# Kernel optimization log

Measured on AMD Instinct MI355X. Metric: run time of the kernel, lower is better.

## Reference

```python
import jax, jax.numpy as jnp
import numpy as np

N = 8192
IN_F = 256
OUT_F = 256


def setup_inputs() -> dict:
    key = jax.random.key(0)
    k_v, k_adj, k1, k2, k3, kb = jax.random.split(key, 6)
    stdv = 1.0 / np.sqrt(OUT_F)
    V = jax.random.normal(k_v, (N, IN_F), dtype=jnp.float32)
    adj = jax.random.randint(k_adj, (N, N), 0, 4, dtype=jnp.int32)
    w1 = jax.random.uniform(k1, (IN_F, OUT_F), jnp.float32, -stdv, stdv)
    w2 = jax.random.uniform(k2, (IN_F, OUT_F), jnp.float32, -stdv, stdv)
    w3 = jax.random.uniform(k3, (IN_F, OUT_F), jnp.float32, -stdv, stdv)
    bias = jax.random.uniform(kb, (OUT_F,), jnp.float32, -stdv, stdv)
    return {"V": V, "adj": adj, "w1": w1, "w2": w2, "w3": w3, "bias": bias}


def reference(V, adj, w1, w2, w3, bias):
    # typed relational GCN: for each edge type k in {1,2,3},
    # aggregate (adj==k) @ (V @ wk), then sum and add bias
    o1 = jnp.matmul((adj == 1).astype(jnp.float32), jnp.matmul(V, w1))
    o2 = jnp.matmul((adj == 2).astype(jnp.float32), jnp.matmul(V, w2))
    o3 = jnp.matmul((adj == 3).astype(jnp.float32), jnp.matmul(V, w3))
    return o1 + o2 + o3 + bias
```

## Files before the change

kernel.cpp:

```cpp
#include <hip/hip_runtime.h>

typedef __attribute__((ext_vector_type(4))) float f32x4;
typedef __attribute__((ext_vector_type(16))) float f32x16;
typedef __attribute__((ext_vector_type(4))) unsigned short u16x4;
typedef __attribute__((ext_vector_type(4))) int i32x4;
typedef __attribute__((ext_vector_type(8))) __bf16 bf16x8;

union FragAB {
  u16x4 u[2];
  i32x4 v;
  bf16x8 f;
};

static __device__ __forceinline__ unsigned short f2bf(float x) {
  union { float f; unsigned u; } v;
  v.f = x;
  unsigned r = v.u + 0x7FFFu + ((v.u >> 16) & 1u);
  return (unsigned short)(r >> 16);
}

#define NN 8192

__global__ __launch_bounds__(256) void k_prep(
    const int* __restrict__ adj, const float* __restrict__ V,
    const float* __restrict__ w1, const float* __restrict__ w2,
    const float* __restrict__ w3, const float* __restrict__ bias,
    unsigned char* __restrict__ adj2b, unsigned short* __restrict__ Vbp,
    unsigned short* __restrict__ Wbp, float* __restrict__ out) {
  int t = blockIdx.x * 256 + threadIdx.x;
  int nT = gridDim.x * 256;
  for (int g = t; g < 16777216; g += nT) {
    i32x4 a = *(const i32x4*)(adj + (size_t)g * 4);
    adj2b[g] = (unsigned char)((a.x & 3) | ((a.y & 3) << 2) |
                               ((a.z & 3) << 4) | ((a.w & 3) << 6));
  }
  for (int g = t; g < 524288; g += nT) {
    int f = g * 4;
    int row = f >> 8, kcol = f & 255;
    f32x4 x = *(const f32x4*)(V + (size_t)f);
    u16x4 h;
    h.x = f2bf(x.x); h.y = f2bf(x.y); h.z = f2bf(x.z); h.w = f2bf(x.w);
    *(u16x4*)(Vbp + (size_t)(kcol >> 3) * 65536 + (size_t)row * 8 + (kcol & 7)) = h;
  }
  for (int e = t; e < 65536; e += nT) {
    int k = e >> 8, n = e & 255;
    Wbp[(size_t)(k >> 3) * 6144 + (size_t)(0 * 256 + n) * 8 + (k & 7)] = f2bf(w1[e]);
  }
  for (int e = t; e < 65536; e += nT) {
    int k = e >> 8, n = e & 255;
    Wbp[(size_t)(k >> 3) * 6144 + (size_t)(1 * 256 + n) * 8 + (k & 7)] = f2bf(w2[e]);
  }
  for (int e = t; e < 65536; e += nT) {
    int k = e >> 8, n = e & 255;
    Wbp[(size_t)(k >> 3) * 6144 + (size_t)(2 * 256 + n) * 8 + (k & 7)] = f2bf(w3[e]);
  }
  for (int g = t; g < 524288; g += nT) {
    *(f32x4*)(out + (size_t)g * 4) = *(const f32x4*)(bias + ((g * 4) & 255));
  }
}

__global__ __launch_bounds__(256) void k_transform(
    const unsigned short* __restrict__ Vbp, const unsigned short* __restrict__ Wbp,
    unsigned short* __restrict__ Bp) {
  int bx = blockIdx.x;
  int rb = bx & 127, nb = bx >> 7;
  int tid = threadIdx.x, lane = tid & 63;
  int wv = tid >> 6;
  int wr = wv >> 1, wc = wv & 1;
  int q = lane >> 4, l16 = lane & 15;

  f32x4 acc[2][4];
#pragma unroll
  for (int i = 0; i < 2; i++)
#pragma unroll
    for (int j = 0; j < 4; j++) acc[i][j] = (f32x4)0.0f;

  int r0 = rb * 64 + wr * 32 + l16;
  int n0 = nb * 128 + wc * 64 + l16;
  const unsigned short* av = Vbp + (size_t)q * 65536 + (size_t)r0 * 8;
  const unsigned short* bv = Wbp + (size_t)q * 6144 + (size_t)n0 * 8;

#pragma unroll 2
  for (int kk = 0; kk < 256; kk += 32) {
    FragAB af[2], bf[4];
#pragma unroll
    for (int mt = 0; mt < 2; mt++)
      af[mt].v = *(const i32x4*)(av + (size_t)(kk >> 3) * 65536 + mt * 128);
#pragma unroll
    for (int nt = 0; nt < 4; nt++)
      bf[nt].v = *(const i32x4*)(bv + (size_t)(kk >> 3) * 6144 + nt * 128);
#pragma unroll
    for (int mt = 0; mt < 2; mt++)
#pragma unroll
      for (int nt = 0; nt < 4; nt++)
        acc[mt][nt] = __builtin_amdgcn_mfma_f32_16x16x32_bf16(
            af[mt].f, bf[nt].f, acc[mt][nt], 0, 0, 0);
  }
#pragma unroll
  for (int mt = 0; mt < 2; mt++)
#pragma unroll
    for (int nt = 0; nt < 4; nt++) {
      int n = n0 + nt * 16;
      int ty = n >> 8, nn = n & 255;
      int j0 = rb * 64 + wr * 32 + mt * 16 + q * 4;
      u16x4 hv;
      hv.x = f2bf(acc[mt][nt].x);
      hv.y = f2bf(acc[mt][nt].y);
      hv.z = f2bf(acc[mt][nt].z);
      hv.w = f2bf(acc[mt][nt].w);
      size_t idx = (size_t)ty * 2097152 + (size_t)(j0 >> 4) * 4096 + nn * 16 + (j0 & 15);
      *(u16x4*)(Bp + idx) = hv;
    }
}

__global__ __launch_bounds__(256, 2) void k_agg(const unsigned* __restrict__ adj2,
                                                const unsigned short* __restrict__ Bp,
                                                float* __restrict__ out) {
  int bx = blockIdx.x;
  int ks = bx & 7, rb = bx >> 3;
  int tid = threadIdx.x, lane = tid & 63;
  int wv = tid >> 6;
  int q = lane >> 5, l32 = lane & 31;
  int qsh = q << 4;

  __shared__ unsigned short ldsB[2][12288];

  f32x16 acc[8];
#pragma unroll
  for (int nt = 0; nt < 8; nt++) acc[nt] = (f32x16)0.0f;

  int row = rb * 128 + wv * 32 + l32;
  const unsigned* ap = adj2 + (size_t)row * 512 + ks * 64;

  const char* Bpb = (const char*)Bp;
  const char* sp[6];
#pragma unroll
  for (int c = 0; c < 6; c++) {
    int ty = c >> 1;
    sp[c] = Bpb + (size_t)ty * 4194304 + (size_t)ks * 524288 + (c & 1) * 4096 +
            tid * 16;
  }

  i32x4 rg[6];
#pragma unroll
  for (int c = 0; c < 6; c++) rg[c] = *(const i32x4*)sp[c];
#pragma unroll
  for (int c = 0; c < 6; c++)
    *(i32x4*)&ldsB[0][c * 2048 + tid * 8] = rg[c];
  unsigned cw = ap[0];
  __syncthreads();

  for (int s = 0; s < 64; ++s) {
    int cur = s & 1;
    if (s < 63) {
#pragma unroll
      for (int c = 0; c < 6; c++)
        rg[c] = *(const i32x4*)(sp[c] + (size_t)(s + 1) * 8192);
    }
    unsigned nxc = (s < 63) ? ap[s + 1] : 0u;
    unsigned w = cw >> qsh;
#pragma unroll
    for (int ty = 0; ty < 3; ty++) {
      FragAB bv[8];
#pragma unroll
      for (int nt = 0; nt < 8; nt++)
        bv[nt].v = *(const i32x4*)&ldsB[cur][ty * 4096 + (nt * 32 + l32) * 16 + q * 8];
      FragAB A;
#pragma unroll
      for (int d = 0; d < 4; d++) {
        unsigned p0 = (w >> (4 * d)) & 3u, p1 = (w >> (4 * d + 2)) & 3u;
        A.v[d] = (int)((p0 == (unsigned)(ty + 1) ? 0x3F80u : 0u) |
                       (p1 == (unsigned)(ty + 1) ? 0x3F800000u : 0u));
      }
#pragma unroll
      for (int nt = 0; nt < 8; nt++)
        acc[nt] = __builtin_amdgcn_mfma_f32_32x32x16_bf16(A.f, bv[nt].f,
                                                          acc[nt], 0, 0, 0);
    }
    if (s < 63) {
#pragma unroll
      for (int c = 0; c < 6; c++)
        *(i32x4*)&ldsB[cur ^ 1][c * 2048 + tid * 8] = rg[c];
    }
    cw = nxc;
    __syncthreads();
  }
#pragma unroll
  for (int nt = 0; nt < 8; nt++) {
    int col = nt * 32 + l32;
    int rowb = rb * 128 + wv * 32 + 4 * q;
#pragma unroll
    for (int r = 0; r < 16; r++) {
      int orow = rowb + (r & 3) + 8 * (r >> 2);
      atomicAdd(out + (size_t)orow * 256 + col, acc[nt][r]);
    }
  }
}

extern "C" void kernel_launch(void* const* d_in, const int* in_sizes, int n_in,
                              void* d_out, int out_size, void* d_ws,
                              size_t ws_size, hipStream_t stream) {
  const float* V = (const float*)d_in[0];
  const int* adj = (const int*)d_in[1];
  const float* w1 = (const float*)d_in[2];
  const float* w2 = (const float*)d_in[3];
  const float* w3 = (const float*)d_in[4];
  const float* bias = (const float*)d_in[5];
  float* out = (float*)d_out;
  unsigned short* Bp = (unsigned short*)d_ws;
  unsigned char* adj2b = (unsigned char*)d_ws + 0xC00000;
  unsigned short* Vbp = (unsigned short*)((char*)d_ws + 0x1C00000);
  unsigned short* Wbp = (unsigned short*)((char*)d_ws + 0x2000000);

  k_prep<<<dim3(2048), dim3(256), 0, stream>>>(adj, V, w1, w2, w3, bias, adj2b,
                                               Vbp, Wbp, out);
  k_transform<<<dim3(768), dim3(256), 0, stream>>>(Vbp, Wbp, Bp);
  k_agg<<<dim3(512), dim3(256), 0, stream>>>((const unsigned*)adj2b, Bp, out);
}
```

Before: 510.2 us.

## Repartition aggregation warps by output columns and pad LDS layout

```diff
diff --git a/kernel.cpp b/kernel.cpp
--- a/kernel.cpp
+++ b/kernel.cpp
@@ -119,82 +119,115 @@
   int bx = blockIdx.x;
   int ks = bx & 7, rb = bx >> 3;
   int tid = threadIdx.x, lane = tid & 63;
-  int wv = tid >> 6;
+  int wn = tid >> 6;
   int q = lane >> 5, l32 = lane & 31;
   int qsh = q << 4;
 
-  __shared__ unsigned short ldsB[2][12288];
-
-  f32x16 acc[8];
-#pragma unroll
-  for (int nt = 0; nt < 8; nt++) acc[nt] = (f32x16)0.0f;
-
-  int row = rb * 128 + wv * 32 + l32;
-  const unsigned* ap = adj2 + (size_t)row * 512 + ks * 64;
+  __shared__ unsigned short ldsB[2][3][256][24];
+
+  f32x16 acc[4][2];
+#pragma unroll
+  for (int mt = 0; mt < 4; mt++)
+#pragma unroll
+    for (int nt = 0; nt < 2; nt++) acc[mt][nt] = (f32x16)0.0f;
+
+  const unsigned* ap = adj2 + (size_t)(rb * 128 + l32) * 512 + ks * 64;
 
   const char* Bpb = (const char*)Bp;
   const char* sp[6];
 #pragma unroll
-  for (int c = 0; c < 6; c++) {
-    int ty = c >> 1;
-    sp[c] = Bpb + (size_t)ty * 4194304 + (size_t)ks * 524288 + (c & 1) * 4096 +
-            tid * 16;
-  }
+  for (int c = 0; c < 6; c++)
+    sp[c] = Bpb + (size_t)(c >> 1) * 4194304 + (size_t)ks * 524288 +
+            (size_t)(c & 1) * 4096 + (size_t)tid * 16;
+
+#define AGG_MT(CC, MT, BV0, BV1, HI)                                           \
+  {                                                                            \
+    unsigned w = (unsigned)(HI ? (CC >> 32) : CC) >> qsh;                      \
+    FragAB A;                                                                  \
+    _Pragma("unroll") for (int d = 0; d < 4; d++) {                            \
+      unsigned p0 = (w >> (4 * d)) & 3u, p1 = (w >> (4 * d + 2)) & 3u;         \
+      A.v[d] = (int)((p0 == ty1 ? 0x3F80u : 0u) |                              \
+                     (p1 == ty1 ? 0x3F800000u : 0u));                          \
+    }                                                                          \
+    acc[MT][0] = __builtin_amdgcn_mfma_f32_32x32x16_bf16(A.f, BV0.f,           \
+                                                         acc[MT][0], 0, 0, 0); \
+    acc[MT][1] = __builtin_amdgcn_mfma_f32_32x32x16_bf16(A.f, BV1.f,           \
+                                                         acc[MT][1], 0, 0, 0); \
+  }
+
+#define AGG_TY(BUF, TY, HI)                                                    \
+  {                                                                            \
+    const unsigned ty1 = TY + 1;                                               \
+    FragAB bv0, bv1;                                                           \
+    bv0.v = *(const i32x4*)&ldsB[BUF][TY][wn * 64 + l32][q * 8];               \
+    bv1.v = *(const i32x4*)&ldsB[BUF][TY][wn * 64 + 32 + l32][q * 8];          \
+    AGG_MT(cc0, 0, bv0, bv1, HI)                                               \
+    AGG_MT(cc1, 1, bv0, bv1, HI)                                               \
+    AGG_MT(cc2, 2, bv0, bv1, HI)                                               \
+    AGG_MT(cc3, 3, bv0, bv1, HI)                                               \
+  }
+
+#define AGG_STEP(BUF, HI)                                                      \
+  AGG_TY(BUF, 0, HI) AGG_TY(BUF, 1, HI) AGG_TY(BUF, 2, HI)
+
+#define AGG_STAGE_WRITE(BUF)                                                   \
+  _Pragma("unroll") for (int c = 0; c < 6; c++)                                \
+      *(i32x4*)&ldsB[BUF][c >> 1][(c & 1) * 128 + (tid >> 1)][(tid & 1) * 8] = \
+          rg[c];
 
   i32x4 rg[6];
 #pragma unroll
   for (int c = 0; c < 6; c++) rg[c] = *(const i32x4*)sp[c];
-#pragma unroll
-  for (int c = 0; c < 6; c++)
-    *(i32x4*)&ldsB[0][c * 2048 + tid * 8] = rg[c];
-  unsigned cw = ap[0];
+  AGG_STAGE_WRITE(0)
+  unsigned long long cc0 = *(const unsigned long long*)(ap);
+  unsigned long long cc1 = *(const unsigned long long*)(ap + 16384);
+  unsigned long long cc2 = *(const unsigned long long*)(ap + 32768);
+  unsigned long long cc3 = *(const unsigned long long*)(ap + 49152);
   __syncthreads();
 
-  for (int s = 0; s < 64; ++s) {
-    int cur = s & 1;
-    if (s < 63) {
+  for (int p = 0; p < 32; ++p) {
+    unsigned long long nx0 = 0, nx1 = 0, nx2 = 0, nx3 = 0;
+    if (p < 31) {
+      nx0 = *(const unsigned long long*)(ap + (p + 1) * 2);
+      nx1 = *(const unsigned long long*)(ap + 16384 + (p + 1) * 2);
+      nx2 = *(const unsigned long long*)(ap + 32768 + (p + 1) * 2);
+      nx3 = *(const unsigned long long*)(ap + 49152 + (p + 1) * 2);
+    }
+    int s0 = 2 * p;
+#pragma unroll
+    for (int c = 0; c < 6; c++)
+      rg[c] = *(const i32x4*)(sp[c] + (size_t)(s0 + 1) * 8192);
+    AGG_STEP(0, 0)
+    AGG_STAGE_WRITE(1)
+    __syncthreads();
+    if (p < 31) {
 #pragma unroll
       for (int c = 0; c < 6; c++)
-        rg[c] = *(const i32x4*)(sp[c] + (size_t)(s + 1) * 8192);
-    }
-    unsigned nxc = (s < 63) ? ap[s + 1] : 0u;
-    unsigned w = cw >> qsh;
-#pragma unroll
-    for (int ty = 0; ty < 3; ty++) {
-      FragAB bv[8];
-#pragma unroll
-      for (int nt = 0; nt < 8; nt++)
-        bv[nt].v = *(const i32x4*)&ldsB[cur][ty * 4096 + (nt * 32 + l32) * 16 + q * 8];
-      FragAB A;
-#pragma unroll
-      for (int d = 0; d < 4; d++) {
-        unsigned p0 = (w >> (4 * d)) & 3u, p1 = (w >> (4 * d + 2)) & 3u;
-        A.v[d] = (int)((p0 == (unsigned)(ty + 1) ? 0x3F80u : 0u) |
-                       (p1 == (unsigned)(ty + 1) ? 0x3F800000u : 0u));
+        rg[c] = *(const i32x4*)(sp[c] + (size_t)(s0 + 2) * 8192);
+    }
+    AGG_STEP(1, 1)
+    if (p < 31) {
+      AGG_STAGE_WRITE(0)
+    }
+    cc0 = nx0; cc1 = nx1; cc2 = nx2; cc3 = nx3;
+    __syncthreads();
+  }
+#pragma unroll
+  for (int mt = 0; mt < 4; mt++)
+#pragma unroll
+    for (int nt = 0; nt < 2; nt++) {
+      int col = wn * 64 + nt * 32 + l32;
+      int rowb = rb * 128 + mt * 32 + 4 * q;
+#pragma unroll
+      for (int r = 0; r < 16; r++) {
+        int row = rowb + (r & 3) + 8 * (r >> 2);
+        atomicAdd(out + (size_t)row * 256 + col, acc[mt][nt][r]);
       }
-#pragma unroll
-      for (int nt = 0; nt < 8; nt++)
-        acc[nt] = __builtin_amdgcn_mfma_f32_32x32x16_bf16(A.f, bv[nt].f,
-                                                          acc[nt], 0, 0, 0);
-    }
-    if (s < 63) {
-#pragma unroll
-      for (int c = 0; c < 6; c++)
-        *(i32x4*)&ldsB[cur ^ 1][c * 2048 + tid * 8] = rg[c];
-    }
-    cw = nxc;
-    __syncthreads();
-  }
-#pragma unroll
-  for (int nt = 0; nt < 8; nt++) {
-    int col = nt * 32 + l32;
-    int rowb = rb * 128 + wv * 32 + 4 * q;
-#pragma unroll
-    for (int r = 0; r < 16; r++) {
-      int orow = rowb + (r & 3) + 8 * (r >> 2);
-      atomicAdd(out + (size_t)orow * 256 + col, acc[nt][r]);
-    }
-  }
+    }
+#undef AGG_MT
+#undef AGG_TY
+#undef AGG_STEP
+#undef AGG_STAGE_WRITE
 }
 
 extern "C" void kernel_launch(void* const* d_in, const int* in_sizes, int n_in,
```

Measured after the change: 538.7 us. 1.06x slower.
